# Kernel optimization log

Measured on AMD Instinct MI355X. Metric: run time of the kernel, lower is better.

Reference implementation:

```python
import jax, jax.numpy as jnp
import numpy as np

EPS = 1e-5

def _bn_relu(x, g, b, m, v):
    # inference batchnorm + relu, NCHW, fused affine
    scale = g * jax.lax.rsqrt(v + EPS)
    shift = b - m * scale
    return jnp.maximum(x * scale[None, :, None, None] + shift[None, :, None, None], 0.0)

def _conv1x1(x, w):
    # x: [B,C,H,W], w: [O,C]
    return jnp.einsum('bchw,oc->bohw', x, w)

def _xcorr_depthwise(search, kernel, padding=0):
    # search: [B,C,Hs,Ws], kernel: [B,C,Hk,Wk]; grouped conv, groups=B*C
    B, C, Hs, Ws = search.shape
    Hk, Wk = kernel.shape[2], kernel.shape[3]
    x = search.reshape(1, B * C, Hs, Ws)
    k = kernel.reshape(B * C, 1, Hk, Wk)
    out = jax.lax.conv_general_dilated(
        x, k, window_strides=(1, 1), padding=[(padding, padding), (padding, padding)],
        feature_group_count=B * C, dimension_numbers=('NCHW', 'OIHW', 'NCHW'))
    return out.reshape(B, C, out.shape[2], out.shape[3])

def setup_inputs():
    key = jax.random.key(0)
    ks = jax.random.split(key, 20)
    B, Cin, HID, COUT = 128, 256, 256, 20
    s = 1.0 / np.sqrt(Cin)
    inp = {
        'kernel': jax.random.normal(ks[0], (B, Cin, 7, 7), jnp.float32),
        'search': jax.random.normal(ks[1], (B, Cin, 31, 31), jnp.float32),
        # conv_kernel branch (1x1 conv weight stored as [O,C]) + BN stats
        'w_k': jax.random.normal(ks[2], (HID, Cin), jnp.float32) * s,
        'g_k': 1.0 + 0.1 * jax.random.normal(ks[3], (HID,), jnp.float32),
        'b_k': 0.1 * jax.random.normal(ks[4], (HID,), jnp.float32),
        'm_k': 0.1 * jax.random.normal(ks[5], (HID,), jnp.float32),
        'v_k': jax.random.uniform(ks[6], (HID,), jnp.float32, 0.5, 1.5),
        # conv_search branch
        'w_s': jax.random.normal(ks[7], (HID, Cin), jnp.float32) * s,
        'g_s': 1.0 + 0.1 * jax.random.normal(ks[8], (HID,), jnp.float32),
        'b_s': 0.1 * jax.random.normal(ks[9], (HID,), jnp.float32),
        'm_s': 0.1 * jax.random.normal(ks[10], (HID,), jnp.float32),
        'v_s': jax.random.uniform(ks[11], (HID,), jnp.float32, 0.5, 1.5),
        # head: conv1(1x1)+BN+ReLU, conv2(1x1, bias)
        'w_h1': jax.random.normal(ks[12], (HID, HID), jnp.float32) * (1.0 / np.sqrt(HID)),
        'g_h': 1.0 + 0.1 * jax.random.normal(ks[13], (HID,), jnp.float32),
        'b_h': 0.1 * jax.random.normal(ks[14], (HID,), jnp.float32),
        'm_h': 0.1 * jax.random.normal(ks[15], (HID,), jnp.float32),
        'v_h': jax.random.uniform(ks[16], (HID,), jnp.float32, 0.5, 1.5),
        'w_h2': jax.random.normal(ks[17], (COUT, HID), jnp.float32) * (1.0 / np.sqrt(HID)),
        'bias_h2': 0.1 * jax.random.normal(ks[18], (COUT,), jnp.float32),
    }
    return inp

def reference(kernel, search, w_k, g_k, b_k, m_k, v_k, w_s, g_s, b_s, m_s, v_s,
              w_h1, g_h, b_h, m_h, v_h, w_h2, bias_h2):
    k = _bn_relu(_conv1x1(kernel, w_k), g_k, b_k, m_k, v_k)   # [B,256,7,7]
    s = _bn_relu(_conv1x1(search, w_s), g_s, b_s, m_s, v_s)   # [B,256,31,31]
    feat = _xcorr_depthwise(s, k, padding=0)                  # [B,256,25,25]
    y = _bn_relu(_conv1x1(feat, w_h1), g_h, b_h, m_h, v_h)
    out = _conv1x1(y, w_h2) + bias_h2[None, :, None, None]    # [B,20,25,25]
    return out
```

## Files before the change

kernel.cpp:

```cpp
#include <hip/hip_runtime.h>
#include <hip/hip_fp16.h>

typedef _Float16 f16;
typedef __attribute__((ext_vector_type(8))) _Float16 f16x8;
typedef __attribute__((ext_vector_type(4))) _Float16 f16x4;
typedef __attribute__((ext_vector_type(4))) float f32x4;

#define MFMA16(a, b, c) __builtin_amdgcn_mfma_f32_16x16x32_f16((a), (b), (c), 0, 0, 0)

#define OFF_WK   0u
#define OFF_WS   131072u
#define OFF_WH1  262144u
#define OFF_W2P  393216u
#define OFF_SH   409600u
#define OFF_S    412672u
#define OFF_KF   63392768u
#define OFF_FEAT 66604032u

__global__ __launch_bounds__(256) void prep_weights(
    const float* __restrict__ wk, const float* __restrict__ gk, const float* __restrict__ bk,
    const float* __restrict__ mk, const float* __restrict__ vk,
    const float* __restrict__ wsr, const float* __restrict__ gs, const float* __restrict__ bs,
    const float* __restrict__ ms, const float* __restrict__ vs,
    const float* __restrict__ wh1, const float* __restrict__ gh, const float* __restrict__ bh,
    const float* __restrict__ mh, const float* __restrict__ vh,
    const float* __restrict__ wh2,
    f16* __restrict__ wk16, f16* __restrict__ ws16, f16* __restrict__ wh116,
    f16* __restrict__ w2p, float* __restrict__ shifts) {
  int o = blockIdx.x;
  int t = threadIdx.x;
  float sck = gk[o] * rsqrtf(vk[o] + 1e-5f);
  float scs = gs[o] * rsqrtf(vs[o] + 1e-5f);
  float sch = gh[o] * rsqrtf(vh[o] + 1e-5f);
  int idx = o * 256 + t;
  wk16[idx]  = (f16)(wk[idx] * sck);
  ws16[idx]  = (f16)(wsr[idx] * scs);
  wh116[idx] = (f16)(wh1[idx] * sch);
  if (o < 32) w2p[idx] = (o < 20) ? (f16)wh2[idx] : (f16)0;
  if (t == 0) {
    shifts[o]       = bk[o] - mk[o] * sck;
    shifts[256 + o] = bs[o] - ms[o] * scs;
    shifts[512 + o] = bh[o] - mh[o] * sch;
  }
}

template <int P>
__global__ __launch_bounds__(256, 4) void conv_f32_allo(
    const float* __restrict__ X, const f16* __restrict__ W,
    const float* __restrict__ shift, f16* __restrict__ out) {
  const int C = 256;
  const int CP = C * P;
  const int LDC8 = 520;
  int n0 = blockIdx.x * 64;
  int t = threadIdx.x;
  int lane = t & 63, wave = t >> 6;
  int fm = lane & 15, kg = lane >> 4;

  __shared__ f16 Bs[32 * LDC8];

  {
    int n4 = (t >> 4) * 4;
    int cb = (t & 15) * 16;
    int gn0 = n0 + n4;
    int bq = gn0 / P;
    int bp = gn0 - bq * P;
    const float* xb = X + (size_t)bq * CP;
    bool safe = (bp + 3 < P);
#pragma unroll
    for (int j = 0; j < 4; ++j) {
      int c0 = cb + j * 4;
      f32x4 col[4];
      if (safe) {
        const float* xp = xb + (size_t)c0 * P + bp;
#pragma unroll
        for (int i = 0; i < 4; ++i) col[i] = *(const f32x4*)(xp + (size_t)i * P);
      } else {
#pragma unroll
        for (int i = 0; i < 4; ++i)
#pragma unroll
          for (int e = 0; e < 4; ++e) {
            int gn = gn0 + e;
            int bqe = gn / P, bpe = gn - bqe * P;
            col[i][e] = X[(size_t)bqe * CP + (size_t)(c0 + i) * P + bpe];
          }
      }
#pragma unroll
      for (int e = 0; e < 4; ++e) {
        f16x4 v;
        v[0] = (f16)col[0][e]; v[1] = (f16)col[1][e];
        v[2] = (f16)col[2][e]; v[3] = (f16)col[3][e];
        *(f16x4*)&Bs[(c0 >> 3) * LDC8 + (n4 + e) * 8 + (c0 & 4)] = v;
      }
    }
  }
  __syncthreads();

  const f16* wp = W + (size_t)(wave * 64 + fm) * C + kg * 8;

  f32x4 acc[4][4] = {};
#pragma unroll
  for (int c0 = 0; c0 < 256; c0 += 32) {
    f16x8 a[4], b[4];
#pragma unroll
    for (int of = 0; of < 4; ++of) a[of] = *(const f16x8*)(wp + (size_t)of * 16 * C + c0);
#pragma unroll
    for (int nf = 0; nf < 4; ++nf)
      b[nf] = *(const f16x8*)&Bs[((c0 >> 3) + kg) * LDC8 + (nf * 16 + fm) * 8];
#pragma unroll
    for (int of = 0; of < 4; ++of)
#pragma unroll
      for (int nf = 0; nf < 4; ++nf)
        acc[of][nf] = MFMA16(a[of], b[nf], acc[of][nf]);
  }

#pragma unroll
  for (int of = 0; of < 4; ++of) {
    int orow = wave * 64 + of * 16 + kg * 4;
#pragma unroll
    for (int nf = 0; nf < 4; ++nf) {
      int n = n0 + nf * 16 + fm;
      f16x4 st;
#pragma unroll
      for (int r = 0; r < 4; ++r)
        st[r] = (f16)fmaxf(acc[of][nf][r] + shift[orow + r], 0.0f);
      *(f16x4*)&out[(size_t)n * 256 + orow] = st;
    }
  }
}

__global__ __launch_bounds__(256) void xcorr_dw_row(
    const f16* __restrict__ S ,
    const f16* __restrict__ K ,
    f16* __restrict__ F ) {
  int id = blockIdx.x;
  int x = id & 7;
  int r = id >> 3;
  int g = r % 7;
  int bq = r / 7;
  int b = bq * 8 + x;

  int wave = threadIdx.x >> 6;
  int lane = threadIdx.x & 63;
  int oi = g * 4 + wave;
  if (oi >= 25) return;

  const f16* Sb = S + (size_t)b * 961 * 256 + lane * 4;
  const f16* Kb = K + (size_t)b * 49 * 256 + lane * 4;

  f32x4 acc[25] = {};

  for (int di = 0; di < 7; ++di) {
    const f16* sp = Sb + (size_t)(oi + di) * 31 * 256;
    f16x4 srow[31];
#pragma unroll
    for (int j = 0; j < 31; ++j) srow[j] = *(const f16x4*)(sp + (size_t)j * 256);
    const f16* kp = Kb + (size_t)di * 7 * 256;
    f16x4 krow[7];
#pragma unroll
    for (int j = 0; j < 7; ++j) krow[j] = *(const f16x4*)(kp + (size_t)j * 256);

#pragma unroll
    for (int dj = 0; dj < 7; ++dj) {
      float k0 = (float)krow[dj][0];
      float k1 = (float)krow[dj][1];
      float k2 = (float)krow[dj][2];
      float k3 = (float)krow[dj][3];
#pragma unroll
      for (int oj = 0; oj < 25; ++oj) {
        f16x4 sv = srow[oj + dj];
        acc[oj][0] += (float)sv[0] * k0;
        acc[oj][1] += (float)sv[1] * k1;
        acc[oj][2] += (float)sv[2] * k2;
        acc[oj][3] += (float)sv[3] * k3;
      }
    }
  }

  f16* Fb = F + ((size_t)b * 625 + (size_t)oi * 25) * 256 + lane * 4;
#pragma unroll
  for (int oj = 0; oj < 25; ++oj) {
    f16x4 o;
#pragma unroll
    for (int e = 0; e < 4; ++e) o[e] = (f16)acc[oj][e];
    *(f16x4*)(Fb + (size_t)oj * 256) = o;
  }
}

__global__ __launch_bounds__(256) void head_fused(
    const f16* __restrict__ Xt ,
    const f16* __restrict__ W1, const float* __restrict__ shift,
    const f16* __restrict__ W2p , const float* __restrict__ bias,
    float* __restrict__ out ) {
  const int C = 256;
  int n0 = blockIdx.x * 64;
  int t = threadIdx.x;
  int lane = t & 63, wave = t >> 6;
  int fm = lane & 15, kg = lane >> 4;

  __shared__ f16 Ys[32][64][8];

  const f16* wp = W1 + (size_t)(wave * 64 + fm) * C + kg * 8;
  const f16* xp = Xt + (size_t)(n0 + fm) * C + kg * 8;

  f32x4 acc[4][4] = {};
#pragma unroll
  for (int c0 = 0; c0 < 256; c0 += 32) {
    f16x8 a[4], b[4];
#pragma unroll
    for (int of = 0; of < 4; ++of) a[of] = *(const f16x8*)(wp + (size_t)of * 16 * C + c0);
#pragma unroll
    for (int nf = 0; nf < 4; ++nf) b[nf] = *(const f16x8*)(xp + (size_t)nf * 16 * C + c0);
#pragma unroll
    for (int of = 0; of < 4; ++of)
#pragma unroll
      for (int nf = 0; nf < 4; ++nf)
        acc[of][nf] = MFMA16(a[of], b[nf], acc[of][nf]);
  }

#pragma unroll
  for (int of = 0; of < 4; ++of) {
    int orow = wave * 64 + of * 16 + kg * 4;
#pragma unroll
    for (int nf = 0; nf < 4; ++nf) {
      int n = nf * 16 + fm;
      f16x4 st;
#pragma unroll
      for (int r = 0; r < 4; ++r)
        st[r] = (f16)fmaxf(acc[of][nf][r] + shift[orow + r], 0.0f);
      *(f16x4*)&Ys[orow >> 3][n][(kg & 1) * 4] = st;
    }
  }
  __syncthreads();

  f32x4 acc2[2] = {};
#pragma unroll
  for (int c0 = 0; c0 < 256; c0 += 32) {
    f16x8 b = *(const f16x8*)&Ys[(c0 >> 3) + kg][wave * 16 + fm][0];
    f16x8 a0 = *(const f16x8*)(W2p + (size_t)fm * C + c0 + kg * 8);
    f16x8 a1 = *(const f16x8*)(W2p + (size_t)(16 + fm) * C + c0 + kg * 8);
    acc2[0] = MFMA16(a0, b, acc2[0]);
    acc2[1] = MFMA16(a1, b, acc2[1]);
  }

  int n = n0 + wave * 16 + fm;
  int bq = n / 625, bp = n - bq * 625;
  float* op = out + (size_t)bq * 12500 + bp;
#pragma unroll
  for (int of = 0; of < 2; ++of) {
#pragma unroll
    for (int r = 0; r < 4; ++r) {
      int o = of * 16 + kg * 4 + r;
      if (o < 20) op[(size_t)o * 625] = acc2[of][r] + bias[o];
    }
  }
}

extern "C" void kernel_launch(void* const* d_in, const int* in_sizes, int n_in,
                              void* d_out, int out_size, void* d_ws, size_t ws_size,
                              hipStream_t stream) {
  const float* kernel_in = (const float*)d_in[0];
  const float* search    = (const float*)d_in[1];
  const float* w_k = (const float*)d_in[2];
  const float* g_k = (const float*)d_in[3];
  const float* b_k = (const float*)d_in[4];
  const float* m_k = (const float*)d_in[5];
  const float* v_k = (const float*)d_in[6];
  const float* w_s = (const float*)d_in[7];
  const float* g_s = (const float*)d_in[8];
  const float* b_s = (const float*)d_in[9];
  const float* m_s = (const float*)d_in[10];
  const float* v_s = (const float*)d_in[11];
  const float* w_h1 = (const float*)d_in[12];
  const float* g_h = (const float*)d_in[13];
  const float* b_h = (const float*)d_in[14];
  const float* m_h = (const float*)d_in[15];
  const float* v_h = (const float*)d_in[16];
  const float* w_h2 = (const float*)d_in[17];
  const float* bias_h2 = (const float*)d_in[18];
  float* out = (float*)d_out;

  char* ws = (char*)d_ws;
  f16* wk16  = (f16*)(ws + OFF_WK);
  f16* ws16  = (f16*)(ws + OFF_WS);
  f16* wh116 = (f16*)(ws + OFF_WH1);
  f16* w2p   = (f16*)(ws + OFF_W2P);
  float* shifts = (float*)(ws + OFF_SH);
  f16* sbuf = (f16*)(ws + OFF_S);
  f16* kbuf = (f16*)(ws + OFF_KF);
  f16* fbuf = (f16*)(ws + OFF_FEAT);

  prep_weights<<<256, 256, 0, stream>>>(w_k, g_k, b_k, m_k, v_k,
                                        w_s, g_s, b_s, m_s, v_s,
                                        w_h1, g_h, b_h, m_h, v_h, w_h2,
                                        wk16, ws16, wh116, w2p, shifts);

  conv_f32_allo<961><<<dim3(1922), 256, 0, stream>>>(
      search, ws16, shifts + 256, sbuf);

  conv_f32_allo<49><<<dim3(98), 256, 0, stream>>>(
      kernel_in, wk16, shifts + 0, kbuf);

  xcorr_dw_row<<<dim3(896), 256, 0, stream>>>(sbuf, kbuf, fbuf);

  head_fused<<<dim3(1250), 256, 0, stream>>>(
      fbuf, wh116, shifts + 512, w2p, bias_h2, out);
}
```

Before: 174.8 us.

## Swizzle LDS tile in 1x1 conv and stage output through LDS for coalesced stores

Replaces the padded LDS layout in the f32-input 1x1 conv with an XOR-swizzled 32KB buffer and remaps the load thread assignment so each thread covers 4 pixels by 4 channels across channel groups. After the MFMA loop, the epilogue writes BN+ReLU results back into the same LDS buffer and then emits 16-byte-per-thread contiguous row stores to global memory, instead of scattered 8-byte stores. This targets LDS bank conflicts and uncoalesced output writes, at the cost of two extra barriers and an LDS round trip.

Measured after the change: 188.5 us. 7.9% more time.

```diff
diff --git a/kernel.cpp b/kernel.cpp
--- a/kernel.cpp
+++ b/kernel.cpp
@@ -50,30 +50,27 @@
     const float* __restrict__ shift, f16* __restrict__ out) {
   const int C = 256;
   const int CP = C * P;
-  const int LDC8 = 520;
   int n0 = blockIdx.x * 64;
   int t = threadIdx.x;
   int lane = t & 63, wave = t >> 6;
   int fm = lane & 15, kg = lane >> 4;
 
-  __shared__ f16 Bs[32 * LDC8];
+  __shared__ char bs[32768];
 
   {
-    int n4 = (t >> 4) * 4;
-    int cb = (t & 15) * 16;
-    int gn0 = n0 + n4;
-    int bq = gn0 / P;
-    int bp = gn0 - bq * P;
-    const float* xb = X + (size_t)bq * CP;
+    int px0 = (t & 15) * 4;
+    int cq  = (t >> 4) * 4;
+    int gn0 = n0 + px0;
+    int bq = gn0 / P, bp = gn0 - bq * P;
+    const float* xb = X + (size_t)bq * CP + bp;
     bool safe = (bp + 3 < P);
 #pragma unroll
     for (int j = 0; j < 4; ++j) {
-      int c0 = cb + j * 4;
+      int cb = j * 64 + cq;
       f32x4 col[4];
       if (safe) {
-        const float* xp = xb + (size_t)c0 * P + bp;
-#pragma unroll
-        for (int i = 0; i < 4; ++i) col[i] = *(const f32x4*)(xp + (size_t)i * P);
+#pragma unroll
+        for (int i = 0; i < 4; ++i) col[i] = *(const f32x4*)(xb + (size_t)(cb + i) * P);
       } else {
 #pragma unroll
         for (int i = 0; i < 4; ++i)
@@ -81,49 +78,70 @@
           for (int e = 0; e < 4; ++e) {
             int gn = gn0 + e;
             int bqe = gn / P, bpe = gn - bqe * P;
-            col[i][e] = X[(size_t)bqe * CP + (size_t)(c0 + i) * P + bpe];
+            col[i][e] = X[(size_t)bqe * CP + (size_t)(cb + i) * P + bpe];
           }
       }
 #pragma unroll
       for (int e = 0; e < 4; ++e) {
+        int ne = px0 + e;
         f16x4 v;
         v[0] = (f16)col[0][e]; v[1] = (f16)col[1][e];
         v[2] = (f16)col[2][e]; v[3] = (f16)col[3][e];
-        *(f16x4*)&Bs[(c0 >> 3) * LDC8 + (n4 + e) * 8 + (c0 & 4)] = v;
+        *(f16x4*)(bs + ((cb >> 3) << 10) + ((ne ^ ((ne >> 3) & 7)) << 4) + ((cb & 7) << 1)) = v;
       }
     }
   }
   __syncthreads();
 
   const f16* wp = W + (size_t)(wave * 64 + fm) * C + kg * 8;
+  int nsw[4];
+#pragma unroll
+  for (int nf = 0; nf < 4; ++nf) {
+    int n = nf * 16 + fm;
+    nsw[nf] = (n ^ ((n >> 3) & 7)) << 4;
+  }
 
   f32x4 acc[4][4] = {};
 #pragma unroll
-  for (int c0 = 0; c0 < 256; c0 += 32) {
+  for (int ci = 0; ci < 8; ++ci) {
     f16x8 a[4], b[4];
 #pragma unroll
-    for (int of = 0; of < 4; ++of) a[of] = *(const f16x8*)(wp + (size_t)of * 16 * C + c0);
+    for (int of = 0; of < 4; ++of)
+      a[of] = *(const f16x8*)(wp + (size_t)of * 16 * C + ci * 32);
 #pragma unroll
     for (int nf = 0; nf < 4; ++nf)
-      b[nf] = *(const f16x8*)&Bs[((c0 >> 3) + kg) * LDC8 + (nf * 16 + fm) * 8];
+      b[nf] = *(const f16x8*)(bs + ((ci * 4 + kg) << 10) + nsw[nf]);
 #pragma unroll
     for (int of = 0; of < 4; ++of)
 #pragma unroll
       for (int nf = 0; nf < 4; ++nf)
         acc[of][nf] = MFMA16(a[of], b[nf], acc[of][nf]);
   }
+  __syncthreads();
 
 #pragma unroll
   for (int of = 0; of < 4; ++of) {
     int orow = wave * 64 + of * 16 + kg * 4;
 #pragma unroll
     for (int nf = 0; nf < 4; ++nf) {
-      int n = n0 + nf * 16 + fm;
       f16x4 st;
 #pragma unroll
       for (int r = 0; r < 4; ++r)
         st[r] = (f16)fmaxf(acc[of][nf][r] + shift[orow + r], 0.0f);
-      *(f16x4*)&out[(size_t)n * 256 + orow] = st;
+      *(f16x4*)(bs + ((orow >> 3) << 10) + nsw[nf] + ((orow & 7) << 1)) = st;
+    }
+  }
+  __syncthreads();
+
+  {
+    int n = t >> 2;
+    int og = (t & 3) * 64;
+    f16* op = out + (size_t)(n0 + n) * 256 + og;
+    int swn = (n ^ ((n >> 3) & 7)) << 4;
+#pragma unroll
+    for (int k = 0; k < 8; ++k) {
+      f16x8 v = *(const f16x8*)(bs + (((og >> 3) + k) << 10) + swn);
+      *(f16x8*)(op + k * 8) = v;
     }
   }
 }
```

## Pipeline NCHW 1x1 conv staging with double-buffered channel chunks and swizzled LDS

Applied to the files above, without the earlier changes.

Replaces the single up-front staging of all 256 input channels into a large LDS tile with a loop over 32-channel chunks. Each chunk is double-buffered in a small swizzled LDS tile, and the next chunk's global loads are issued before the MFMAs run, so memory loads can overlap compute. Per-thread loads become contiguous 4-pixel rows across two channels, and the shift loads are vectorised. The smaller LDS footprint should raise occupancy, at the cost of a barrier every chunk and dropping the explicit occupancy hint from launch bounds.

After: 175.2 us. Within noise of the previous version (+0.2%).

```diff
diff --git a/kernel.cpp b/kernel.cpp
--- a/kernel.cpp
+++ b/kernel.cpp
@@ -4,6 +4,7 @@
 typedef _Float16 f16;
 typedef __attribute__((ext_vector_type(8))) _Float16 f16x8;
 typedef __attribute__((ext_vector_type(4))) _Float16 f16x4;
+typedef __attribute__((ext_vector_type(2))) _Float16 f16x2;
 typedef __attribute__((ext_vector_type(4))) float f32x4;
 
 #define MFMA16(a, b, c) __builtin_amdgcn_mfma_f32_16x16x32_f16((a), (b), (c), 0, 0, 0)
@@ -44,68 +45,97 @@
   }
 }
 
+__device__ __forceinline__ int pi_row(int q, int r) {
+  return (q ^ (r << 2)) + (r << 4);
+}
+
 template <int P>
-__global__ __launch_bounds__(256, 4) void conv_f32_allo(
+__global__ __launch_bounds__(256) void conv_nchw(
     const float* __restrict__ X, const f16* __restrict__ W,
     const float* __restrict__ shift, f16* __restrict__ out) {
   const int C = 256;
-  const int CP = C * P;
-  const int LDC8 = 520;
   int n0 = blockIdx.x * 64;
   int t = threadIdx.x;
   int lane = t & 63, wave = t >> 6;
   int fm = lane & 15, kg = lane >> 4;
 
-  __shared__ f16 Bs[32 * LDC8];
-
+  __shared__ f16 Bs[2][64 * 40];
+
+  int b0 = n0 / P, bp0 = n0 - b0 * P;
+  bool safe = (bp0 + 64 <= P);
+
+  int px = (t & 15) * 4;
+  int cpr = (t >> 4) * 2;
+  const float* xb = X + ((size_t)b0 * C) * P + bp0 + px;
+
+  int ub[4], up[4];
+  if (!safe) {
+#pragma unroll
+    for (int e = 0; e < 4; ++e) {
+      int gn = n0 + px + e;
+      ub[e] = gn / P;
+      up[e] = gn - ub[e] * P;
+    }
+  }
+
+  int wrow[4];
+#pragma unroll
+  for (int e = 0; e < 4; ++e) wrow[e] = pi_row(t & 15, e);
+
+  int rrow[4];
+#pragma unroll
+  for (int nf = 0; nf < 4; ++nf) rrow[nf] = pi_row(nf * 4 + (fm >> 2), fm & 3);
+
+  const f16* wp = W + (size_t)(wave * 64 + fm) * C + kg * 8;
+
+  f32x4 r0, r1;
   {
-    int n4 = (t >> 4) * 4;
-    int cb = (t & 15) * 16;
-    int gn0 = n0 + n4;
-    int bq = gn0 / P;
-    int bp = gn0 - bq * P;
-    const float* xb = X + (size_t)bq * CP;
-    bool safe = (bp + 3 < P);
-#pragma unroll
-    for (int j = 0; j < 4; ++j) {
-      int c0 = cb + j * 4;
-      f32x4 col[4];
+    int cl = cpr;
+    if (safe) {
+      r0 = *(const f32x4*)(xb + (size_t)cl * P);
+      r1 = *(const f32x4*)(xb + (size_t)(cl + 1) * P);
+    } else {
+#pragma unroll
+      for (int e = 0; e < 4; ++e) {
+        r0[e] = X[((size_t)ub[e] * C + cl) * P + up[e]];
+        r1[e] = X[((size_t)ub[e] * C + cl + 1) * P + up[e]];
+      }
+    }
+  }
+
+  f32x4 acc[4][4] = {};
+#pragma unroll
+  for (int ci = 0; ci < 8; ++ci) {
+    f16* buf = Bs[ci & 1];
+#pragma unroll
+    for (int e = 0; e < 4; ++e) {
+      f16x2 v;
+      v[0] = (f16)r0[e];
+      v[1] = (f16)r1[e];
+      *(f16x2*)&buf[wrow[e] * 40 + cpr] = v;
+    }
+    if (ci < 7) {
+      int cl = (ci + 1) * 32 + cpr;
       if (safe) {
-        const float* xp = xb + (size_t)c0 * P + bp;
-#pragma unroll
-        for (int i = 0; i < 4; ++i) col[i] = *(const f32x4*)(xp + (size_t)i * P);
+        r0 = *(const f32x4*)(xb + (size_t)cl * P);
+        r1 = *(const f32x4*)(xb + (size_t)(cl + 1) * P);
       } else {
 #pragma unroll
-        for (int i = 0; i < 4; ++i)
-#pragma unroll
-          for (int e = 0; e < 4; ++e) {
-            int gn = gn0 + e;
-            int bqe = gn / P, bpe = gn - bqe * P;
-            col[i][e] = X[(size_t)bqe * CP + (size_t)(c0 + i) * P + bpe];
-          }
+        for (int e = 0; e < 4; ++e) {
+          r0[e] = X[((size_t)ub[e] * C + cl) * P + up[e]];
+          r1[e] = X[((size_t)ub[e] * C + cl + 1) * P + up[e]];
+        }
       }
-#pragma unroll
-      for (int e = 0; e < 4; ++e) {
-        f16x4 v;
-        v[0] = (f16)col[0][e]; v[1] = (f16)col[1][e];
-        v[2] = (f16)col[2][e]; v[3] = (f16)col[3][e];
-        *(f16x4*)&Bs[(c0 >> 3) * LDC8 + (n4 + e) * 8 + (c0 & 4)] = v;
-      }
-    }
-  }
-  __syncthreads();
-
-  const f16* wp = W + (size_t)(wave * 64 + fm) * C + kg * 8;
-
-  f32x4 acc[4][4] = {};
-#pragma unroll
-  for (int c0 = 0; c0 < 256; c0 += 32) {
+    }
+    __syncthreads();
+
     f16x8 a[4], b[4];
 #pragma unroll
-    for (int of = 0; of < 4; ++of) a[of] = *(const f16x8*)(wp + (size_t)of * 16 * C + c0);
+    for (int of = 0; of < 4; ++of)
+      a[of] = *(const f16x8*)(wp + (size_t)of * 16 * C + ci * 32);
 #pragma unroll
     for (int nf = 0; nf < 4; ++nf)
-      b[nf] = *(const f16x8*)&Bs[((c0 >> 3) + kg) * LDC8 + (nf * 16 + fm) * 8];
+      b[nf] = *(const f16x8*)&buf[rrow[nf] * 40 + kg * 8];
 #pragma unroll
     for (int of = 0; of < 4; ++of)
 #pragma unroll
@@ -116,14 +146,15 @@
 #pragma unroll
   for (int of = 0; of < 4; ++of) {
     int orow = wave * 64 + of * 16 + kg * 4;
+    f32x4 sh = *(const f32x4*)(shift + orow);
 #pragma unroll
     for (int nf = 0; nf < 4; ++nf) {
       int n = n0 + nf * 16 + fm;
       f16x4 st;
 #pragma unroll
       for (int r = 0; r < 4; ++r)
-        st[r] = (f16)fmaxf(acc[of][nf][r] + shift[orow + r], 0.0f);
-      *(f16x4*)&out[(size_t)n * 256 + orow] = st;
+        st[r] = (f16)fmaxf(acc[of][nf][r] + sh[r], 0.0f);
+      *(f16x4*)(out + (size_t)n * C + orow) = st;
     }
   }
 }
@@ -294,11 +325,8 @@
                                         w_h1, g_h, b_h, m_h, v_h, w_h2,
                                         wk16, ws16, wh116, w2p, shifts);
 
-  conv_f32_allo<961><<<dim3(1922), 256, 0, stream>>>(
-      search, ws16, shifts + 256, sbuf);
-
-  conv_f32_allo<49><<<dim3(98), 256, 0, stream>>>(
-      kernel_in, wk16, shifts + 0, kbuf);
+  conv_nchw<961><<<dim3(1922), 256, 0, stream>>>(search, ws16, shifts + 256, sbuf);
+  conv_nchw<49><<<dim3(98), 256, 0, stream>>>(kernel_in, wk16, shifts + 0, kbuf);
 
   xcorr_dw_row<<<dim3(896), 256, 0, stream>>>(sbuf, kbuf, fbuf);
 
```
